# Kernel tuning notes

Hardware: AMD Instinct MI355X
Metric: run time of the kernel (lower is better)

Reference implementation:

```python
import jax, jax.numpy as jnp
import numpy as np

N, K, C_S, C_Z, C_G, N_RBF = 1024, 16, 256, 128, 16, 64
EPS = 1e-8


def _ln(x, g, b, eps=1e-5):
    m = x.mean(-1, keepdims=True)
    v = jnp.mean((x - m) ** 2, -1, keepdims=True)
    return (x - m) * jax.lax.rsqrt(v + eps) * g + b


def _rbf(D, D_count=N_RBF, D_min=0.0, D_max=20.0):
    mu = jnp.linspace(D_min, D_max, D_count, dtype=D.dtype)
    sigma = (D_max - D_min) / D_count
    return jnp.exp(-(((D[..., None] - mu) / sigma) ** 2))


def setup_inputs() -> dict:
    key = jax.random.key(0)
    ks = jax.random.split(key, 20)
    node_features = jax.random.normal(ks[0], (N, C_S), jnp.float32)
    trans = jax.random.normal(ks[1], (N, 3), jnp.float32) * 5.0  # CA translations, Angstrom-ish
    edge_features = jax.random.normal(ks[2], (N * K, C_Z), jnp.float32)
    # sparse graph laid out as K neighbors per node: dst = node i repeated K times
    src = jax.random.randint(ks[3], (N * K,), 0, N)
    dst = jnp.repeat(jnp.arange(N), K)
    edge_index = jnp.stack([src, dst]).astype(jnp.int64)
    batch = jnp.zeros((N,), jnp.int64)
    res_mask = jnp.ones((N,), bool)
    w = lambda k, i, o: jax.random.normal(k, (i, o), jnp.float32) * 0.02
    return {
        "node_features": node_features, "trans": trans, "edge_features": edge_features,
        "ln_g": jnp.ones((C_Z,), jnp.float32), "ln_b": jnp.zeros((C_Z,), jnp.float32),
        "Wl": w(ks[4], C_S, C_G), "bl": jnp.zeros((C_G,), jnp.float32),
        "Wr": w(ks[5], C_S, C_G), "br": jnp.zeros((C_G,), jnp.float32),
        "Wep": w(ks[6], C_Z, C_Z), "bep": jnp.zeros((C_Z,), jnp.float32),
        "Weg": w(ks[7], C_Z, C_Z), "beg": jnp.zeros((C_Z,), jnp.float32),
        "Wdg": w(ks[8], C_G * C_G, C_Z), "bdg": jnp.zeros((C_Z,), jnp.float32),
        "Wdp": w(ks[9], N_RBF, C_Z), "bdp": jnp.zeros((C_Z,), jnp.float32),
        "lno_g": jnp.ones((C_Z,), jnp.float32), "lno_b": jnp.zeros((C_Z,), jnp.float32),
        "Wout": w(ks[10], C_Z, C_Z), "bout": jnp.zeros((C_Z,), jnp.float32),
        "Wog": w(ks[11], C_Z, C_Z), "bog": jnp.zeros((C_Z,), jnp.float32),
        "edge_index": edge_index, "batch": batch, "res_mask": res_mask,
    }


def reference(node_features, trans, edge_features, ln_g, ln_b, Wl, bl, Wr, br,
              Wep, bep, Weg, beg, Wdg, bdg, Wdp, bdp, lno_g, lno_b, Wout, bout,
              Wog, bog, edge_index, batch, res_mask):
    n = node_features.shape[0]
    src = edge_index[0].reshape(n, K)              # neighbor indices per node [N,K]
    # sparse -> kNN: edges are grouped K per destination node
    knn_feats = edge_features.reshape(n, K, C_Z)
    knn_mask = res_mask[src] & res_mask[:, None]   # [N,K]
    z = _ln(knn_feats, ln_g, ln_b)
    # outer-product node gating
    nl = node_features @ Wl + bl                   # [N,c_g]
    nr = node_features @ Wr + br
    a = nl[src]                                    # [N,K,c_g]
    b = nr[src]
    edge3 = a[:, :, None, :, None] * b[:, None, :, None, :]   # [N,K,K,c_g,c_g]
    gate3 = edge3.reshape(n, K, K, C_G * C_G) @ Wdg + bdg     # [N,K,K,c_z]
    # RBF distance features among the K neighbors of each node
    t = trans[src]                                 # [N,K,3]
    d = jnp.linalg.norm(t[:, :, None, :] - t[:, None, :, :] + EPS, axis=-1)  # [N,K,K]
    df = _rbf(d) @ Wdp + bdp                       # [N,K,K,c_z]
    m2 = (knn_mask[:, :, None] & knn_mask[:, None, :]).astype(df.dtype)
    e3 = jax.nn.sigmoid(gate3) * df * m2[..., None]
    # gated edge projection
    e2 = jax.nn.sigmoid(z @ Weg + beg) * (z @ Wep + bep)      # [N,K,c_z]
    # triangle matmul: per channel c, [K,K] @ [K]
    upd = jnp.einsum('njkc,nkc->njc', e3, e2)                 # [N,K,c_z]
    upd = _ln(upd, lno_g, lno_b) @ Wout + bout
    upd = upd * jax.nn.sigmoid(z @ Wog + bog)
    # kNN -> sparse scatter back (masked)
    out = (upd * knn_mask[..., None].astype(upd.dtype)).reshape(n * K, C_Z)
    return out
```

## Files before the change

### kernel.cpp

```cpp
#include <hip/hip_runtime.h>
#include <math.h>

#define KNN  16
#define CZ   128
#define CG   16
#define CS   256
#define NN   1024

typedef __attribute__((ext_vector_type(8))) _Float16 half8;
typedef __attribute__((ext_vector_type(4))) _Float16 half4;
typedef __attribute__((ext_vector_type(2))) _Float16 half2v;
typedef __attribute__((ext_vector_type(4))) float f4_t;

#define MFMA16x32(A, B, C) __builtin_amdgcn_mfma_f32_16x16x32_f16((A), (B), (C), 0, 0, 0)
#define MFMA16x16(A, B, C) __builtin_amdgcn_mfma_f32_16x16x16f16((A), (B), (C), 0, 0, 0)

union U8 { half2v h[4]; half8 v; };
union U4 { half2v h[2]; half4 v; };

__device__ __forceinline__ half2v pk2(float x, float y) {
    auto t = __builtin_amdgcn_cvt_pkrtz(x, y);
    half2v r;
    __builtin_memcpy(&r, &t, 4);
    return r;
}
__device__ __forceinline__ float sig_(float x) {
    return __builtin_amdgcn_rcpf(1.0f + __expf(-x));
}

__global__ __launch_bounds__(256) void prep_kernel(
    const float* __restrict__ Wdp, const float* __restrict__ Wdg,
    const float* __restrict__ Wout, const float* __restrict__ Wep,
    const float* __restrict__ Weg, const float* __restrict__ Wog,
    _Float16* __restrict__ pk,
    const float* __restrict__ nf,
    const float* __restrict__ Wl, const float* __restrict__ bl,
    const float* __restrict__ Wr, const float* __restrict__ br,
    float* __restrict__ nlo, float* __restrict__ nro) {
    int b = blockIdx.x, tid = threadIdx.x;
    if (b < 416) {
        int gid = b * 256 + tid;
        float val;
        if (gid >= 8192 && gid < 40960) {
            int o = gid - 8192;
            int i = o & 3, l = (o >> 2) & 63, ct = (o >> 8) & 7, q = o >> 11;
            int row = (4 * (l >> 4) + i) * 16 + q;
            int col = ct * 16 + (l & 15);
            val = Wdg[row * CZ + col];
        } else {
            const float* srcw;
            int o;
            if (gid < 8192)        { srcw = Wdp;  o = gid; }
            else if (gid < 57344)  { srcw = Wout; o = gid - 40960; }
            else if (gid < 73728)  { srcw = Wep;  o = gid - 57344; }
            else if (gid < 90112)  { srcw = Weg;  o = gid - 73728; }
            else                   { srcw = Wog;  o = gid - 90112; }
            int t = o & 7, l = (o >> 3) & 63, ct = (o >> 9) & 7, s = o >> 12;
            int row = s * 32 + (l >> 4) * 8 + t;
            int col = ct * 16 + (l & 15);
            val = srcw[row * CZ + col];
        }
        pk[gid] = (_Float16)val;
    } else {
        int grp = tid >> 6, lane = tid & 63;
        int n = (b - 416) * 4 + grp;
        int p = lane & 15, seg = lane >> 4;
        float accl = (seg == 0) ? bl[p] : 0.0f;
        float accr = (seg == 0) ? br[p] : 0.0f;
        const float* rw = nf + n * CS + seg * 64;
        for (int i = 0; i < 64; ++i) {
            float v = rw[i];
            int s = seg * 64 + i;
            accl += v * Wl[s * CG + p];
            accr += v * Wr[s * CG + p];
        }
        accl += __shfl_xor(accl, 16); accl += __shfl_xor(accl, 32);
        accr += __shfl_xor(accr, 16); accr += __shfl_xor(accr, 32);
        if (lane < 16) { nlo[n * CG + lane] = accl; nro[n * CG + lane] = accr; }
    }
}

__global__ __launch_bounds__(256) void main_kernel(
    const float* __restrict__ trans, const float* __restrict__ ef,
    const float* __restrict__ lng, const float* __restrict__ lnb,
    const float* __restrict__ nl, const float* __restrict__ nr,
    const float* __restrict__ bep, const float* __restrict__ beg,
    const float* __restrict__ bog,
    const _Float16* __restrict__ Wepp, const _Float16* __restrict__ Wegp,
    const _Float16* __restrict__ Wogp,
    const _Float16* __restrict__ Wdg2, const float* __restrict__ bdg,
    const _Float16* __restrict__ Wdpp, const float* __restrict__ bdp,
    const float* __restrict__ lnog, const float* __restrict__ lnob,
    const _Float16* __restrict__ Woutp, const float* __restrict__ bout,
    const int* __restrict__ src, const int* __restrict__ resmask,
    float* __restrict__ out) {
    __shared__ _Float16 s_zu[16 * 136];
    __shared__ float s_t[64];
    __shared__ float s_km[16];
    __shared__ int   s_src[16];
    __shared__ float s_a[256];
    __shared__ float s_b[16 * 20];
    __shared__ _Float16 s_T[4 * 4096];

    int n = blockIdx.x, tid = threadIdx.x;
    if (tid < 16) {
        int sv = src[n * KNN + tid];
        s_src[tid] = sv;
        s_km[tid] = (resmask[sv] != 0 && resmask[n] != 0) ? 1.0f : 0.0f;
        s_t[tid * 4 + 0] = trans[sv * 3 + 0];
        s_t[tid * 4 + 1] = trans[sv * 3 + 1];
        s_t[tid * 4 + 2] = trans[sv * 3 + 2];
    }
    __syncthreads();
    {
        int j = tid >> 4, p = tid & 15;
        int sv = s_src[j];
        s_a[j * 16 + p] = nl[sv * CG + p];
        s_b[j * 20 + p] = nr[sv * CG + p];
    }
    {
        int r = tid >> 4, seg = tid & 15;
        const float* row = ef + ((size_t)n * KNN + r) * CZ + seg * 8;
        f4_t x0 = *(const f4_t*)row;
        f4_t x1 = *(const f4_t*)(row + 4);
        float s = x0.x + x0.y + x0.z + x0.w + x1.x + x1.y + x1.z + x1.w;
        float q = x0.x * x0.x + x0.y * x0.y + x0.z * x0.z + x0.w * x0.w
                + x1.x * x1.x + x1.y * x1.y + x1.z * x1.z + x1.w * x1.w;
        #pragma unroll
        for (int m = 1; m < 16; m <<= 1) { s += __shfl_xor(s, m); q += __shfl_xor(q, m); }
        float mean = s * (1.0f / CZ);
        float var  = q * (1.0f / CZ) - mean * mean;
        float rs   = __builtin_amdgcn_rsqf(var + 1e-5f);
        int col = seg * 8;
        f4_t g0 = *(const f4_t*)(lng + col), g1 = *(const f4_t*)(lng + col + 4);
        f4_t b0 = *(const f4_t*)(lnb + col), b1 = *(const f4_t*)(lnb + col + 4);
        U8 zu;
        zu.h[0] = pk2((x0.x - mean) * rs * g0.x + b0.x, (x0.y - mean) * rs * g0.y + b0.y);
        zu.h[1] = pk2((x0.z - mean) * rs * g0.z + b0.z, (x0.w - mean) * rs * g0.w + b0.w);
        zu.h[2] = pk2((x1.x - mean) * rs * g1.x + b1.x, (x1.y - mean) * rs * g1.y + b1.y);
        zu.h[3] = pk2((x1.z - mean) * rs * g1.z + b1.z, (x1.w - mean) * rs * g1.w + b1.w);
        *(half8*)&s_zu[r * 136 + col] = zu.v;
    }
    __syncthreads();

    int wv = tid >> 6, lane = tid & 63, l15 = lane & 15, quad = lane >> 4;

    half8 Az[4];
    #pragma unroll
    for (int st = 0; st < 4; ++st)
        Az[st] = *(const half8*)&s_zu[l15 * 136 + st * 32 + quad * 8];
    f4_t e2f[2], ggf[2];
    #pragma unroll
    for (int cc = 0; cc < 2; ++cc) {
        int ct = wv * 2 + cc;
        int c = ct * 16 + l15;
        float vep = bep[c], veg = beg[c], vog = bog[c];
        f4_t aep = {vep, vep, vep, vep};
        f4_t aeg = {veg, veg, veg, veg};
        f4_t aog = {vog, vog, vog, vog};
        #pragma unroll
        for (int st = 0; st < 4; ++st) {
            int off = ((st * 8 + ct) * 64 + lane) * 8;
            half8 wep_ = *(const half8*)(Wepp + off);
            half8 weg_ = *(const half8*)(Wegp + off);
            half8 wog_ = *(const half8*)(Wogp + off);
            aep = MFMA16x32(Az[st], wep_, aep);
            aeg = MFMA16x32(Az[st], weg_, aeg);
            aog = MFMA16x32(Az[st], wog_, aog);
        }
        #pragma unroll
        for (int rr = 0; rr < 4; ++rr) {
            e2f[cc][rr] = sig_(aeg[rr]) * aep[rr] * s_km[quad * 4 + rr];
            ggf[cc][rr] = sig_(aog[rr]);
        }
    }
    __syncthreads();

    half8 Bdp_[2][2];
    #pragma unroll
    for (int st = 0; st < 2; ++st)
        #pragma unroll
        for (int cc = 0; cc < 2; ++cc)
            Bdp_[st][cc] = *(const half8*)(Wdpp + ((st * 8 + wv * 2 + cc) * 64 + lane) * 8);

    float bdgv[2], bdpv[2];
    #pragma unroll
    for (int cc = 0; cc < 2; ++cc) {
        int c = (wv * 2 + cc) * 16 + l15;
        bdgv[cc] = bdg[c];
        bdpv[cc] = bdp[c];
    }

    half4 Aa, Ab;
    {
        f4_t av = *(const f4_t*)&s_a[l15 * 16 + 4 * quad];
        U4 u; u.h[0] = pk2(av.x, av.y); u.h[1] = pk2(av.z, av.w);
        Aa = u.v;
        f4_t bv = *(const f4_t*)&s_b[l15 * 20 + 4 * quad];
        U4 w; w.h[0] = pk2(bv.x, bv.y); w.h[1] = pk2(bv.z, bv.w);
        Ab = w.v;
    }

    float tkx = s_t[l15 * 4 + 0], tky = s_t[l15 * 4 + 1], tkz = s_t[l15 * 4 + 2];
    const float MUS = 20.0f / 63.0f;
    const float ISG = 1.0f / 0.3125f;
    float rIS[2];
    #pragma unroll
    for (int st = 0; st < 2; ++st)
        rIS[st] = (float)(st * 32 + quad * 8) * (MUS * ISG);

    _Float16* Tw = s_T + wv * 4096;
    int jl_base = 4 * (quad & 1);
    int myh = quad >> 1;

    for (int h = 0; h < 2; ++h) {
        #pragma unroll
        for (int ctl = 0; ctl < 2; ++ctl) {
            int ct = wv * 2 + ctl;
            #pragma unroll
            for (int qb = 0; qb < 4; ++qb) {
                f4_t tq[4];
                #pragma unroll
                for (int qq = 0; qq < 4; ++qq) {
                    half4 Bw = *(const half4*)(Wdg2 + (((4 * qb + qq) * 8 + ct) * 64 + lane) * 4);
                    f4_t z = {0.f, 0.f, 0.f, 0.f};
                    tq[qq] = MFMA16x16(Aa, Bw, z);
                }
                if (myh == h) {
                    #pragma unroll
                    for (int rr = 0; rr < 4; ++rr) {
                        U4 u;
                        u.h[0] = pk2(tq[0][rr], tq[1][rr]);
                        u.h[1] = pk2(tq[2][rr], tq[3][rr]);
                        int jl = jl_base + rr;
                        *(half4*)&Tw[((jl * 2 + ctl) * 64 + l15 + 16 * qb) * 4] = u.v;
                    }
                }
            }
        }

        for (int j = 8 * h; j < 8 * h + 8; ++j) {
            float dx = s_t[j * 4 + 0] - tkx + 1e-8f;
            float dy = s_t[j * 4 + 1] - tky + 1e-8f;
            float dz = s_t[j * 4 + 2] - tkz + 1e-8f;
            float dI = sqrtf(dx * dx + dy * dy + dz * dz) * ISG;

            half8 ar[2];
            #pragma unroll
            for (int st = 0; st < 2; ++st) {
                U8 cv;
                float base0 = dI - rIS[st];
                #pragma unroll
                for (int tt = 0; tt < 4; ++tt) {
                    float u0 = base0 - (float)(2 * tt) * (MUS * ISG);
                    float u1 = u0 - (MUS * ISG);
                    cv.h[tt] = pk2(__expf(-u0 * u0), __expf(-u1 * u1));
                }
                ar[st] = cv.v;
            }
            f4_t accd[2], accg[2];
            #pragma unroll
            for (int cc = 0; cc < 2; ++cc) {
                f4_t z = {bdpv[cc], bdpv[cc], bdpv[cc], bdpv[cc]};
                z = MFMA16x32(ar[0], Bdp_[0][cc], z);
                z = MFMA16x32(ar[1], Bdp_[1][cc], z);
                accd[cc] = z;
                half4 Bt = *(const half4*)&Tw[(((j & 7) * 2 + cc) * 64 + l15 + 16 * quad) * 4];
                f4_t g = {bdgv[cc], bdgv[cc], bdgv[cc], bdgv[cc]};
                accg[cc] = MFMA16x16(Ab, Bt, g);
            }
            float kmj = s_km[j];
            #pragma unroll
            for (int cc = 0; cc < 2; ++cc) {
                float part = 0.f;
                #pragma unroll
                for (int rr = 0; rr < 4; ++rr)
                    part += sig_(accg[cc][rr]) * accd[cc][rr] * e2f[cc][rr];
                part += __shfl_xor(part, 16);
                part += __shfl_xor(part, 32);
                if (lane < 16)
                    s_zu[j * 136 + (wv * 2 + cc) * 16 + lane] = (_Float16)(part * kmj);
            }
        }
    }
    __syncthreads();

    #pragma unroll
    for (int rr2 = 0; rr2 < 4; ++rr2) {
        int rj = wv * 4 + rr2;
        float x0 = (float)s_zu[rj * 136 + lane];
        float x1 = (float)s_zu[rj * 136 + 64 + lane];
        float sm = x0 + x1, sq = x0 * x0 + x1 * x1;
        #pragma unroll
        for (int m = 1; m < 64; m <<= 1) {
            sm += __shfl_xor(sm, m);
            sq += __shfl_xor(sq, m);
        }
        float mean = sm * (1.0f / CZ);
        float var  = sq * (1.0f / CZ) - mean * mean;
        float rsv  = __builtin_amdgcn_rsqf(var + 1e-5f);
        float h0 = (x0 - mean) * rsv * lnog[lane] + lnob[lane];
        float h1 = (x1 - mean) * rsv * lnog[64 + lane] + lnob[64 + lane];
        s_zu[rj * 136 + lane]      = (_Float16)h0;
        s_zu[rj * 136 + 64 + lane] = (_Float16)h1;
    }
    __syncthreads();

    half8 Aw[4];
    #pragma unroll
    for (int st = 0; st < 4; ++st)
        Aw[st] = *(const half8*)&s_zu[l15 * 136 + st * 32 + quad * 8];
    #pragma unroll
    for (int cc = 0; cc < 2; ++cc) {
        int ct = wv * 2 + cc;
        int c = ct * 16 + l15;
        float bo = bout[c];
        f4_t acc = {bo, bo, bo, bo};
        #pragma unroll
        for (int st = 0; st < 4; ++st) {
            half8 bw = *(const half8*)(Woutp + ((st * 8 + ct) * 64 + lane) * 8);
            acc = MFMA16x32(Aw[st], bw, acc);
        }
        #pragma unroll
        for (int rr = 0; rr < 4; ++rr) {
            int row = quad * 4 + rr;
            size_t oi = (size_t)(n * KNN + row) * CZ + c;
            out[oi] = acc[rr] * ggf[cc][rr] * s_km[row];
        }
    }
}

extern "C" void kernel_launch(void* const* d_in, const int* in_sizes, int n_in,
                              void* d_out, int out_size, void* d_ws, size_t ws_size,
                              hipStream_t stream) {
    const float* node_features = (const float*)d_in[0];
    const float* trans         = (const float*)d_in[1];
    const float* edge_features = (const float*)d_in[2];
    const float* ln_g  = (const float*)d_in[3];
    const float* ln_b  = (const float*)d_in[4];
    const float* Wl    = (const float*)d_in[5];
    const float* bl    = (const float*)d_in[6];
    const float* Wr    = (const float*)d_in[7];
    const float* br    = (const float*)d_in[8];
    const float* Wep   = (const float*)d_in[9];
    const float* bep   = (const float*)d_in[10];
    const float* Weg   = (const float*)d_in[11];
    const float* beg   = (const float*)d_in[12];
    const float* Wdg   = (const float*)d_in[13];
    const float* bdg   = (const float*)d_in[14];
    const float* Wdp   = (const float*)d_in[15];
    const float* bdp   = (const float*)d_in[16];
    const float* lno_g = (const float*)d_in[17];
    const float* lno_b = (const float*)d_in[18];
    const float* Wout  = (const float*)d_in[19];
    const float* bout  = (const float*)d_in[20];
    const float* Wog   = (const float*)d_in[21];
    const float* bog   = (const float*)d_in[22];
    const int* edge_index = (const int*)d_in[23];
    const int* resmask    = (const int*)d_in[25];

    float* ws = (float*)d_ws;
    float* nl = ws;
    float* nr = nl + NN * CG;
    _Float16* pk = (_Float16*)(nr + NN * CG);
    _Float16* Wdpp  = pk;
    _Float16* Wdg2  = pk + 8192;
    _Float16* Woutp = pk + 40960;
    _Float16* Wepp  = pk + 57344;
    _Float16* Wegp  = pk + 73728;
    _Float16* Wogp  = pk + 90112;
    const int* src = edge_index;

    prep_kernel<<<672, 256, 0, stream>>>(
        Wdp, Wdg, Wout, Wep, Weg, Wog, pk,
        node_features, Wl, bl, Wr, br, nl, nr);
    main_kernel<<<NN, 256, 0, stream>>>(
        trans, edge_features, ln_g, ln_b, nl, nr,
        bep, beg, bog, Wepp, Wegp, Wogp,
        Wdg2, bdg, Wdpp, bdp, lno_g, lno_b,
        Woutp, bout, src, resmask, (float*)d_out);
}
```

Before: 172.8 us.

## Split RBF feature generation across waves and reduce partials through LDS

```diff
diff --git a/kernel.cpp b/kernel.cpp
--- a/kernel.cpp
+++ b/kernel.cpp
@@ -100,7 +100,9 @@
     __shared__ int   s_src[16];
     __shared__ float s_a[256];
     __shared__ float s_b[16 * 20];
-    __shared__ _Float16 s_T[4 * 4096];
+    __shared__ _Float16 s_T[4 * 2048];
+    __shared__ _Float16 s_fr[8 * 64 * 8];
+    __shared__ _Float16 s_part[16 * CZ * 4];
 
     int n = blockIdx.x, tid = threadIdx.x;
     if (tid < 16) {
@@ -176,6 +178,15 @@
     }
     __syncthreads();
 
+    {
+        U8 g;
+        g.h[0] = pk2(ggf[0][0], ggf[0][1]);
+        g.h[1] = pk2(ggf[0][2], ggf[0][3]);
+        g.h[2] = pk2(ggf[1][0], ggf[1][1]);
+        g.h[3] = pk2(ggf[1][2], ggf[1][3]);
+        *(half8*)&s_zu[tid * 8] = g.v;
+    }
+
     half8 Bdp_[2][2];
     #pragma unroll
     for (int st = 0; st < 2; ++st)
@@ -209,11 +220,9 @@
     for (int st = 0; st < 2; ++st)
         rIS[st] = (float)(st * 32 + quad * 8) * (MUS * ISG);
 
-    _Float16* Tw = s_T + wv * 4096;
-    int jl_base = 4 * (quad & 1);
-    int myh = quad >> 1;
-
-    for (int h = 0; h < 2; ++h) {
+    _Float16* Tw = s_T + wv * 2048;
+
+    for (int Q = 0; Q < 4; ++Q) {
         #pragma unroll
         for (int ctl = 0; ctl < 2; ++ctl) {
             int ct = wv * 2 + ctl;
@@ -226,70 +235,79 @@
                     f4_t z = {0.f, 0.f, 0.f, 0.f};
                     tq[qq] = MFMA16x16(Aa, Bw, z);
                 }
-                if (myh == h) {
+                if (quad == Q) {
                     #pragma unroll
                     for (int rr = 0; rr < 4; ++rr) {
                         U4 u;
                         u.h[0] = pk2(tq[0][rr], tq[1][rr]);
                         u.h[1] = pk2(tq[2][rr], tq[3][rr]);
-                        int jl = jl_base + rr;
-                        *(half4*)&Tw[((jl * 2 + ctl) * 64 + l15 + 16 * qb) * 4] = u.v;
+                        *(half4*)&Tw[((rr * 2 + ctl) * 64 + l15 + 16 * qb) * 4] = u.v;
                     }
                 }
             }
         }
 
-        for (int j = 8 * h; j < 8 * h + 8; ++j) {
+        #pragma unroll
+        for (int uu = 0; uu < 2; ++uu) {
+            int u = wv * 2 + uu;
+            int m = u >> 1, st = u & 1;
+            int j = 4 * Q + m;
             float dx = s_t[j * 4 + 0] - tkx + 1e-8f;
             float dy = s_t[j * 4 + 1] - tky + 1e-8f;
             float dz = s_t[j * 4 + 2] - tkz + 1e-8f;
             float dI = sqrtf(dx * dx + dy * dy + dz * dz) * ISG;
-
-            half8 ar[2];
+            float base0 = dI - rIS[st];
+            U8 cv;
             #pragma unroll
-            for (int st = 0; st < 2; ++st) {
-                U8 cv;
-                float base0 = dI - rIS[st];
-                #pragma unroll
-                for (int tt = 0; tt < 4; ++tt) {
-                    float u0 = base0 - (float)(2 * tt) * (MUS * ISG);
-                    float u1 = u0 - (MUS * ISG);
-                    cv.h[tt] = pk2(__expf(-u0 * u0), __expf(-u1 * u1));
-                }
-                ar[st] = cv.v;
+            for (int tt = 0; tt < 4; ++tt) {
+                float u0 = base0 - (float)(2 * tt) * (MUS * ISG);
+                float u1 = u0 - (MUS * ISG);
+                cv.h[tt] = pk2(__expf(-u0 * u0), __expf(-u1 * u1));
             }
+            *(half8*)&s_fr[(u * 64 + lane) * 8] = cv.v;
+        }
+        __syncthreads();
+
+        for (int m = 0; m < 4; ++m) {
+            int j = 4 * Q + m;
+            half8 ar0 = *(const half8*)&s_fr[((m * 2 + 0) * 64 + lane) * 8];
+            half8 ar1 = *(const half8*)&s_fr[((m * 2 + 1) * 64 + lane) * 8];
             f4_t accd[2], accg[2];
             #pragma unroll
             for (int cc = 0; cc < 2; ++cc) {
                 f4_t z = {bdpv[cc], bdpv[cc], bdpv[cc], bdpv[cc]};
-                z = MFMA16x32(ar[0], Bdp_[0][cc], z);
-                z = MFMA16x32(ar[1], Bdp_[1][cc], z);
+                z = MFMA16x32(ar0, Bdp_[0][cc], z);
+                z = MFMA16x32(ar1, Bdp_[1][cc], z);
                 accd[cc] = z;
-                half4 Bt = *(const half4*)&Tw[(((j & 7) * 2 + cc) * 64 + l15 + 16 * quad) * 4];
+                half4 Bt = *(const half4*)&Tw[((m * 2 + cc) * 64 + l15 + 16 * quad) * 4];
                 f4_t g = {bdgv[cc], bdgv[cc], bdgv[cc], bdgv[cc]};
                 accg[cc] = MFMA16x16(Ab, Bt, g);
             }
-            float kmj = s_km[j];
             #pragma unroll
             for (int cc = 0; cc < 2; ++cc) {
-                float part = 0.f;
+                float pr = 0.f;
                 #pragma unroll
                 for (int rr = 0; rr < 4; ++rr)
-                    part += sig_(accg[cc][rr]) * accd[cc][rr] * e2f[cc][rr];
-                part += __shfl_xor(part, 16);
-                part += __shfl_xor(part, 32);
-                if (lane < 16)
-                    s_zu[j * 136 + (wv * 2 + cc) * 16 + lane] = (_Float16)(part * kmj);
+                    pr += sig_(accg[cc][rr]) * accd[cc][rr] * e2f[cc][rr];
+                s_part[(j * CZ + (wv * 2 + cc) * 16 + l15) * 4 + quad] = (_Float16)pr;
             }
         }
-    }
+        __syncthreads();
+    }
+
+    half8 gv = *(const half8*)&s_zu[tid * 8];
     __syncthreads();
 
     #pragma unroll
     for (int rr2 = 0; rr2 < 4; ++rr2) {
         int rj = wv * 4 + rr2;
-        float x0 = (float)s_zu[rj * 136 + lane];
-        float x1 = (float)s_zu[rj * 136 + 64 + lane];
+        U4 p0, p1;
+        p0.v = *(const half4*)&s_part[(rj * CZ + lane) * 4];
+        p1.v = *(const half4*)&s_part[(rj * CZ + lane + 64) * 4];
+        half2v t0 = p0.h[0] + p0.h[1];
+        half2v t1 = p1.h[0] + p1.h[1];
+        float x0 = (float)t0[0] + (float)t0[1];
+        float x1 = (float)t1[0] + (float)t1[1];
         float sm = x0 + x1, sq = x0 * x0 + x1 * x1;
         #pragma unroll
         for (int m = 1; m < 64; m <<= 1) {
@@ -325,7 +343,7 @@
         for (int rr = 0; rr < 4; ++rr) {
             int row = quad * 4 + rr;
             size_t oi = (size_t)(n * KNN + row) * CZ + c;
-            out[oi] = acc[rr] * ggf[cc][rr] * s_km[row];
+            out[oi] = acc[rr] * (float)gv[cc * 4 + rr] * s_km[row];
         }
     }
 }
```

Measured after the change: 161.5 us. 6.6% less time.
